# Kernel optimization log

Hardware: AMD Instinct MI355X
Metric: run time of the kernel (lower is better)

## Reference

```python
import jax, jax.numpy as jnp
import numpy as np

H = 2048
B, L, S = 4, 4096, 10

def setup_inputs() -> dict:
    key = jax.random.key(0)
    k1, k2, k3, k4, k5, k6 = jax.random.split(key, 6)
    scale = 1.0 / np.sqrt(H)
    return {
        "h_english": jax.random.normal(k1, (B, L, H), dtype=jnp.float32),
        "h_lojban": jax.random.normal(k2, (B, S, H), dtype=jnp.float32),
        "w_q": jax.random.normal(k3, (H, H), dtype=jnp.float32) * scale,
        "w_k": jax.random.normal(k4, (H, H), dtype=jnp.float32) * scale,
        "w_v": jax.random.normal(k5, (H, H), dtype=jnp.float32) * scale,
        "w_o": jax.random.normal(k6, (H, H), dtype=jnp.float32) * scale,
        "alpha": jnp.float32(0.1),
    }

def reference(h_english, h_lojban, w_q, w_k, w_v, w_o, alpha):
    h = h_english.shape[-1]
    # torch Linear: y = x @ W^T
    q = jnp.einsum('blh,oh->blo', h_english, w_q)   # [B,L,H]
    k = jnp.einsum('bsh,oh->bso', h_lojban, w_k)    # [B,S,H]
    v = jnp.einsum('bsh,oh->bso', h_lojban, w_v)    # [B,S,H]
    scores = jnp.einsum('blh,bsh->bls', q, k) / jnp.sqrt(jnp.float32(h))  # [B,L,S]
    probs = jax.nn.softmax(scores, axis=-1)
    context = jnp.einsum('bls,bsh->blh', probs, v)  # [B,L,H]
    delta = jnp.einsum('blh,oh->blo', context, w_o)
    return h_english + alpha * delta
```

## Files before the change

kernel.cpp:

```cpp
#include <hip/hip_runtime.h>

#define SDIM 10
#define HDIM 2048
#define LDIM 4096
#define BDIM 4

#define KSCALE 0.02209708691207961f

__global__ __launch_bounds__(256) void kv_kernel(
    const float* __restrict__ h_l, const float* __restrict__ w_k,
    const float* __restrict__ w_v, float* __restrict__ k_out,
    float* __restrict__ v_out) {
  const int b = blockIdx.y;
  const int wave = threadIdx.x >> 6;
  const int lane = threadIdx.x & 63;
  const int opair = blockIdx.x * 4 + wave;
  const int o0 = opair * 2;

  const float4* hl4 = (const float4*)(h_l + (size_t)b * SDIM * HDIM);
  const float4* wk0 = (const float4*)(w_k + (size_t)o0 * HDIM);
  const float4* wk1 = (const float4*)(w_k + (size_t)(o0 + 1) * HDIM);
  const float4* wv0 = (const float4*)(w_v + (size_t)o0 * HDIM);
  const float4* wv1 = (const float4*)(w_v + (size_t)(o0 + 1) * HDIM);

  float ak0[SDIM], ak1[SDIM], av0[SDIM], av1[SDIM];
#pragma unroll
  for (int s = 0; s < SDIM; s++) { ak0[s] = ak1[s] = av0[s] = av1[s] = 0.f; }

#pragma unroll
  for (int j = 0; j < 8; j++) {
    const int idx = j * 64 + lane;
    const float4 a0 = wk0[idx], a1 = wk1[idx];
    const float4 c0 = wv0[idx], c1 = wv1[idx];
#pragma unroll
    for (int s = 0; s < SDIM; s++) {
      const float4 h = hl4[s * 512 + idx];
      ak0[s] += a0.x * h.x + a0.y * h.y + a0.z * h.z + a0.w * h.w;
      ak1[s] += a1.x * h.x + a1.y * h.y + a1.z * h.z + a1.w * h.w;
      av0[s] += c0.x * h.x + c0.y * h.y + c0.z * h.z + c0.w * h.w;
      av1[s] += c1.x * h.x + c1.y * h.y + c1.z * h.z + c1.w * h.w;
    }
  }
#pragma unroll
  for (int s = 0; s < SDIM; s++) {
#pragma unroll
    for (int d = 1; d < 64; d <<= 1) {
      ak0[s] += __shfl_xor(ak0[s], d);
      ak1[s] += __shfl_xor(ak1[s], d);
      av0[s] += __shfl_xor(av0[s], d);
      av1[s] += __shfl_xor(av1[s], d);
    }
  }
  if (lane == 0) {
#pragma unroll
    for (int s = 0; s < SDIM; s++) {
      const size_t base = ((size_t)b * SDIM + s) * HDIM + o0;
      k_out[base]     = ak0[s];
      k_out[base + 1] = ak1[s];
      v_out[base]     = av0[s];
      v_out[base + 1] = av1[s];
    }
  }
}

#define OSPLIT 16
__global__ __launch_bounds__(256) void kk_part_kernel(
    const float* __restrict__ k_in, const float* __restrict__ w_q,
    float* __restrict__ part) {
  const int b = blockIdx.z;
  const int oc = blockIdx.y >> 1;
  const int s0 = (blockIdx.y & 1) * 5;
  const int f4 = blockIdx.x * 256 + threadIdx.x;

  __shared__ float ksh[5 * 128];
  for (int idx = threadIdx.x; idx < 5 * 128; idx += 256) {
    const int s = idx >> 7, oo = idx & 127;
    ksh[idx] = k_in[((size_t)b * SDIM + s0 + s) * HDIM + oc * 128 + oo];
  }
  __syncthreads();

  float4 acc[5];
#pragma unroll
  for (int s = 0; s < 5; s++) acc[s] = make_float4(0.f, 0.f, 0.f, 0.f);

  const float4* wq4 = (const float4*)w_q;
  for (int oo = 0; oo < 128; oo++) {
    const float4 w = wq4[(size_t)(oc * 128 + oo) * 512 + f4];
#pragma unroll
    for (int s = 0; s < 5; s++) {
      const float kv = ksh[s * 128 + oo];
      acc[s].x += kv * w.x; acc[s].y += kv * w.y;
      acc[s].z += kv * w.z; acc[s].w += kv * w.w;
    }
  }
#pragma unroll
  for (int s = 0; s < 5; s++) {
    ((float4*)part)[(((size_t)oc * BDIM + b) * SDIM + s0 + s) * 512 + f4] = acc[s];
  }
}

__global__ __launch_bounds__(256) void kk_reduce_kernel(
    const float* __restrict__ part, float* __restrict__ kk_out) {
  const int t = blockIdx.x * 256 + threadIdx.x;
  const float4* p4 = (const float4*)part;
  float4 acc = make_float4(0.f, 0.f, 0.f, 0.f);
#pragma unroll
  for (int p = 0; p < OSPLIT; p++) {
    const float4 v = p4[(size_t)p * 20480 + t];
    acc.x += v.x; acc.y += v.y; acc.z += v.z; acc.w += v.w;
  }
  ((float4*)kk_out)[t] = acc;
}

__global__ __launch_bounds__(256) void vo_kernel(
    const float* __restrict__ v_in, const float* __restrict__ w_o,
    float* __restrict__ vo_out) {
  const int b = blockIdx.y;
  const int wave = threadIdx.x >> 6;
  const int lane = threadIdx.x & 63;
  const int opair = blockIdx.x * 4 + wave;
  const int o0 = opair * 2;

  const float4* vb4 = (const float4*)(v_in + (size_t)b * SDIM * HDIM);
  const float4* wo0 = (const float4*)(w_o + (size_t)o0 * HDIM);
  const float4* wo1 = (const float4*)(w_o + (size_t)(o0 + 1) * HDIM);

  float a0[SDIM], a1[SDIM];
#pragma unroll
  for (int s = 0; s < SDIM; s++) { a0[s] = a1[s] = 0.f; }

#pragma unroll
  for (int j = 0; j < 8; j++) {
    const int idx = j * 64 + lane;
    const float4 w0 = wo0[idx], w1 = wo1[idx];
#pragma unroll
    for (int s = 0; s < SDIM; s++) {
      const float4 h = vb4[s * 512 + idx];
      a0[s] += w0.x * h.x + w0.y * h.y + w0.z * h.z + w0.w * h.w;
      a1[s] += w1.x * h.x + w1.y * h.y + w1.z * h.z + w1.w * h.w;
    }
  }
#pragma unroll
  for (int s = 0; s < SDIM; s++) {
#pragma unroll
    for (int d = 1; d < 64; d <<= 1) {
      a0[s] += __shfl_xor(a0[s], d);
      a1[s] += __shfl_xor(a1[s], d);
    }
  }
  if (lane == 0) {
#pragma unroll
    for (int s = 0; s < SDIM; s++) {
      const size_t base = ((size_t)b * SDIM + s) * HDIM + o0;
      vo_out[base]     = a0[s];
      vo_out[base + 1] = a1[s];
    }
  }
}

__global__ __launch_bounds__(256) void attn_kernel(
    const float* __restrict__ h_e, const float* __restrict__ kk,
    const float* __restrict__ vo, const float* __restrict__ alpha_p,
    float* __restrict__ out) {
  const int b = blockIdx.y;
  const int wave = threadIdx.x >> 6;
  const int lane = threadIdx.x & 63;
  const int row0 = blockIdx.x * 8 + wave * 2;
  const float alpha = *alpha_p;
  const float4* kkb = (const float4*)(kk + (size_t)b * SDIM * HDIM);
  const float4* vob = (const float4*)(vo + (size_t)b * SDIM * HDIM);
  const size_t rowbase = ((size_t)b * LDIM + row0) * HDIM;

  float4 he[2][8];
#pragma unroll
  for (int r = 0; r < 2; r++) {
    const float4* src = (const float4*)(h_e + rowbase + (size_t)r * HDIM);
#pragma unroll
    for (int i = 0; i < 8; i++) he[r][i] = src[i * 64 + lane];
  }

  float acc[2][SDIM];
#pragma unroll
  for (int r = 0; r < 2; r++)
#pragma unroll
    for (int s = 0; s < SDIM; s++) acc[r][s] = 0.f;

#pragma unroll
  for (int i = 0; i < 8; i++) {
#pragma unroll
    for (int s = 0; s < SDIM; s++) {
      const float4 kv = kkb[s * 512 + i * 64 + lane];
#pragma unroll
      for (int r = 0; r < 2; r++)
        acc[r][s] += he[r][i].x * kv.x + he[r][i].y * kv.y +
                     he[r][i].z * kv.z + he[r][i].w * kv.w;
    }
  }

#pragma unroll
  for (int r = 0; r < 2; r++)
#pragma unroll
    for (int s = 0; s < SDIM; s++) {
      float v = acc[r][s];
      v += __shfl_xor(v, 1);
      v += __shfl_xor(v, 2);
      v += __shfl_xor(v, 4);
      v += __shfl_xor(v, 8);
      v += __shfl_xor(v, 16);
      v += __shfl_xor(v, 32);
      acc[r][s] = v * KSCALE;
    }

#pragma unroll
  for (int r = 0; r < 2; r++) {
    float m = acc[r][0];
#pragma unroll
    for (int s = 1; s < SDIM; s++) m = fmaxf(m, acc[r][s]);
    float sum = 0.f;
#pragma unroll
    for (int s = 0; s < SDIM; s++) {
      acc[r][s] = __expf(acc[r][s] - m);
      sum += acc[r][s];
    }
    const float inv = alpha / sum;
#pragma unroll
    for (int s = 0; s < SDIM; s++) acc[r][s] *= inv;
  }

#pragma unroll
  for (int i = 0; i < 8; i++) {
    float4 o4[2];
#pragma unroll
    for (int r = 0; r < 2; r++) o4[r] = he[r][i];
#pragma unroll
    for (int s = 0; s < SDIM; s++) {
      const float4 vv = vob[s * 512 + i * 64 + lane];
#pragma unroll
      for (int r = 0; r < 2; r++) {
        o4[r].x += acc[r][s] * vv.x;
        o4[r].y += acc[r][s] * vv.y;
        o4[r].z += acc[r][s] * vv.z;
        o4[r].w += acc[r][s] * vv.w;
      }
    }
#pragma unroll
    for (int r = 0; r < 2; r++)
      ((float4*)(out + rowbase + (size_t)r * HDIM))[i * 64 + lane] = o4[r];
  }
}

extern "C" void kernel_launch(void* const* d_in, const int* in_sizes, int n_in,
                              void* d_out, int out_size, void* d_ws, size_t ws_size,
                              hipStream_t stream) {
  const float* h_e   = (const float*)d_in[0];
  const float* h_l   = (const float*)d_in[1];
  const float* w_q   = (const float*)d_in[2];
  const float* w_k   = (const float*)d_in[3];
  const float* w_v   = (const float*)d_in[4];
  const float* w_o   = (const float*)d_in[5];
  const float* alpha = (const float*)d_in[6];
  float* out = (float*)d_out;

  float* ws      = (float*)d_ws;
  float* k_ws    = ws;
  float* v_ws    = ws + 81920;
  float* kk_ws   = ws + 163840;
  float* vo_ws   = ws + 245760;
  float* part_ws = ws + 327680;

  kv_kernel<<<dim3(256, BDIM), 256, 0, stream>>>(h_l, w_k, w_v, k_ws, v_ws);
  kk_part_kernel<<<dim3(2, 32, BDIM), 256, 0, stream>>>(k_ws, w_q, part_ws);
  vo_kernel<<<dim3(256, BDIM), 256, 0, stream>>>(v_ws, w_o, vo_ws);
  kk_reduce_kernel<<<80, 256, 0, stream>>>(part_ws, kk_ws);
  attn_kernel<<<dim3(512, BDIM), 256, 0, stream>>>(h_e, kk_ws, vo_ws, alpha, out);
}
```

Before: 417.8 us.

## Batch-merge KV/VO projections and stage attention K/V chunks through LDS

The kv and vo kernels now compute one output column for all four batches per wave instead of two columns for one batch. Each weight row is read once rather than once per batch, which cuts weight traffic. The attention kernel stages the kk and vo vectors into double-buffered LDS with global_load_lds and block-level barriers, replacing the per-wave redundant global loads. This adds synchronisation and LDS pressure, and the larger accumulator arrays raise register use.

New measurement: 556.9 us. 33.3% more time.

```diff
diff --git a/kernel.cpp b/kernel.cpp
--- a/kernel.cpp
+++ b/kernel.cpp
@@ -7,59 +7,57 @@
 
 #define KSCALE 0.02209708691207961f
 
-__global__ __launch_bounds__(256) void kv_kernel(
+__global__ __launch_bounds__(256, 2) void kv_kernel(
     const float* __restrict__ h_l, const float* __restrict__ w_k,
     const float* __restrict__ w_v, float* __restrict__ k_out,
     float* __restrict__ v_out) {
-  const int b = blockIdx.y;
   const int wave = threadIdx.x >> 6;
   const int lane = threadIdx.x & 63;
-  const int opair = blockIdx.x * 4 + wave;
-  const int o0 = opair * 2;
-
-  const float4* hl4 = (const float4*)(h_l + (size_t)b * SDIM * HDIM);
-  const float4* wk0 = (const float4*)(w_k + (size_t)o0 * HDIM);
-  const float4* wk1 = (const float4*)(w_k + (size_t)(o0 + 1) * HDIM);
-  const float4* wv0 = (const float4*)(w_v + (size_t)o0 * HDIM);
-  const float4* wv1 = (const float4*)(w_v + (size_t)(o0 + 1) * HDIM);
-
-  float ak0[SDIM], ak1[SDIM], av0[SDIM], av1[SDIM];
-#pragma unroll
-  for (int s = 0; s < SDIM; s++) { ak0[s] = ak1[s] = av0[s] = av1[s] = 0.f; }
+  const int o = blockIdx.x * 4 + wave;
+
+  const float4* wk = (const float4*)(w_k + (size_t)o * HDIM);
+  const float4* wv = (const float4*)(w_v + (size_t)o * HDIM);
+  const float4* hl4 = (const float4*)h_l;
+
+  float ak[BDIM][SDIM], av[BDIM][SDIM];
+#pragma unroll
+  for (int b = 0; b < BDIM; b++)
+#pragma unroll
+    for (int s = 0; s < SDIM; s++) { ak[b][s] = 0.f; av[b][s] = 0.f; }
 
 #pragma unroll
   for (int j = 0; j < 8; j++) {
     const int idx = j * 64 + lane;
-    const float4 a0 = wk0[idx], a1 = wk1[idx];
-    const float4 c0 = wv0[idx], c1 = wv1[idx];
+    const float4 a = wk[idx];
+    const float4 c = wv[idx];
+#pragma unroll
+    for (int b = 0; b < BDIM; b++)
+#pragma unroll
+      for (int s = 0; s < SDIM; s++) {
+        const float4 h = hl4[(size_t)(b * SDIM + s) * 512 + idx];
+        ak[b][s] += a.x * h.x + a.y * h.y + a.z * h.z + a.w * h.w;
+        av[b][s] += c.x * h.x + c.y * h.y + c.z * h.z + c.w * h.w;
+      }
+  }
+#pragma unroll
+  for (int b = 0; b < BDIM; b++)
 #pragma unroll
     for (int s = 0; s < SDIM; s++) {
-      const float4 h = hl4[s * 512 + idx];
-      ak0[s] += a0.x * h.x + a0.y * h.y + a0.z * h.z + a0.w * h.w;
-      ak1[s] += a1.x * h.x + a1.y * h.y + a1.z * h.z + a1.w * h.w;
-      av0[s] += c0.x * h.x + c0.y * h.y + c0.z * h.z + c0.w * h.w;
-      av1[s] += c1.x * h.x + c1.y * h.y + c1.z * h.z + c1.w * h.w;
-    }
-  }
-#pragma unroll
-  for (int s = 0; s < SDIM; s++) {
-#pragma unroll
-    for (int d = 1; d < 64; d <<= 1) {
-      ak0[s] += __shfl_xor(ak0[s], d);
-      ak1[s] += __shfl_xor(ak1[s], d);
-      av0[s] += __shfl_xor(av0[s], d);
-      av1[s] += __shfl_xor(av1[s], d);
-    }
-  }
+#pragma unroll
+      for (int d = 1; d < 64; d <<= 1) {
+        ak[b][s] += __shfl_xor(ak[b][s], d);
+        av[b][s] += __shfl_xor(av[b][s], d);
+      }
+    }
   if (lane == 0) {
 #pragma unroll
-    for (int s = 0; s < SDIM; s++) {
-      const size_t base = ((size_t)b * SDIM + s) * HDIM + o0;
-      k_out[base]     = ak0[s];
-      k_out[base + 1] = ak1[s];
-      v_out[base]     = av0[s];
-      v_out[base + 1] = av1[s];
-    }
+    for (int b = 0; b < BDIM; b++)
+#pragma unroll
+      for (int s = 0; s < SDIM; s++) {
+        const size_t base = ((size_t)b * SDIM + s) * HDIM + o;
+        k_out[base] = ak[b][s];
+        v_out[base] = av[b][s];
+      }
   }
 }
 
@@ -112,65 +110,80 @@
   ((float4*)kk_out)[t] = acc;
 }
 
-__global__ __launch_bounds__(256) void vo_kernel(
+__global__ __launch_bounds__(256, 2) void vo_kernel(
     const float* __restrict__ v_in, const float* __restrict__ w_o,
     float* __restrict__ vo_out) {
-  const int b = blockIdx.y;
   const int wave = threadIdx.x >> 6;
   const int lane = threadIdx.x & 63;
-  const int opair = blockIdx.x * 4 + wave;
-  const int o0 = opair * 2;
-
-  const float4* vb4 = (const float4*)(v_in + (size_t)b * SDIM * HDIM);
-  const float4* wo0 = (const float4*)(w_o + (size_t)o0 * HDIM);
-  const float4* wo1 = (const float4*)(w_o + (size_t)(o0 + 1) * HDIM);
-
-  float a0[SDIM], a1[SDIM];
-#pragma unroll
-  for (int s = 0; s < SDIM; s++) { a0[s] = a1[s] = 0.f; }
+  const int o = blockIdx.x * 4 + wave;
+
+  const float4* wo = (const float4*)(w_o + (size_t)o * HDIM);
+  const float4* vb4 = (const float4*)v_in;
+
+  float a[BDIM][SDIM];
+#pragma unroll
+  for (int b = 0; b < BDIM; b++)
+#pragma unroll
+    for (int s = 0; s < SDIM; s++) a[b][s] = 0.f;
 
 #pragma unroll
   for (int j = 0; j < 8; j++) {
     const int idx = j * 64 + lane;
-    const float4 w0 = wo0[idx], w1 = wo1[idx];
+    const float4 w = wo[idx];
+#pragma unroll
+    for (int b = 0; b < BDIM; b++)
+#pragma unroll
+      for (int s = 0; s < SDIM; s++) {
+        const float4 h = vb4[(size_t)(b * SDIM + s) * 512 + idx];
+        a[b][s] += w.x * h.x + w.y * h.y + w.z * h.z + w.w * h.w;
+      }
+  }
+#pragma unroll
+  for (int b = 0; b < BDIM; b++)
 #pragma unroll
     for (int s = 0; s < SDIM; s++) {
-      const float4 h = vb4[s * 512 + idx];
-      a0[s] += w0.x * h.x + w0.y * h.y + w0.z * h.z + w0.w * h.w;
-      a1[s] += w1.x * h.x + w1.y * h.y + w1.z * h.z + w1.w * h.w;
-    }
-  }
-#pragma unroll
-  for (int s = 0; s < SDIM; s++) {
-#pragma unroll
-    for (int d = 1; d < 64; d <<= 1) {
-      a0[s] += __shfl_xor(a0[s], d);
-      a1[s] += __shfl_xor(a1[s], d);
-    }
-  }
+#pragma unroll
+      for (int d = 1; d < 64; d <<= 1) a[b][s] += __shfl_xor(a[b][s], d);
+    }
   if (lane == 0) {
 #pragma unroll
-    for (int s = 0; s < SDIM; s++) {
-      const size_t base = ((size_t)b * SDIM + s) * HDIM + o0;
-      vo_out[base]     = a0[s];
-      vo_out[base + 1] = a1[s];
-    }
-  }
-}
-
-__global__ __launch_bounds__(256) void attn_kernel(
+    for (int b = 0; b < BDIM; b++)
+#pragma unroll
+      for (int s = 0; s < SDIM; s++)
+        vo_out[((size_t)b * SDIM + s) * HDIM + o] = a[b][s];
+  }
+}
+
+__device__ __forceinline__ void stage_chunk(const float4* __restrict__ src,
+                                            float4* lds_base, int j, int tid,
+                                            int wave) {
+#pragma unroll
+  for (int k = 0; k < 5; k++) {
+    const int idx = k * 256 + tid;
+    const float4* g = src + (size_t)(idx >> 7) * 512 + j * 128 + (idx & 127);
+    float4* l = lds_base + k * 256 + (wave << 6);
+    __builtin_amdgcn_global_load_lds(
+        (const __attribute__((address_space(1))) void*)g,
+        (__attribute__((address_space(3))) void*)l, 16, 0, 0);
+  }
+}
+
+__global__ __launch_bounds__(256, 3) void attn_kernel(
     const float* __restrict__ h_e, const float* __restrict__ kk,
     const float* __restrict__ vo, const float* __restrict__ alpha_p,
     float* __restrict__ out) {
   const int b = blockIdx.y;
   const int wave = threadIdx.x >> 6;
   const int lane = threadIdx.x & 63;
+  const int tid = threadIdx.x;
   const int row0 = blockIdx.x * 8 + wave * 2;
   const float alpha = *alpha_p;
   const float4* kkb = (const float4*)(kk + (size_t)b * SDIM * HDIM);
   const float4* vob = (const float4*)(vo + (size_t)b * SDIM * HDIM);
   const size_t rowbase = ((size_t)b * LDIM + row0) * HDIM;
 
+  __shared__ float4 lds[2][SDIM * 128];
+
   float4 he[2][8];
 #pragma unroll
   for (int r = 0; r < 2; r++) {
@@ -185,15 +198,23 @@
 #pragma unroll
     for (int s = 0; s < SDIM; s++) acc[r][s] = 0.f;
 
-#pragma unroll
-  for (int i = 0; i < 8; i++) {
-#pragma unroll
-    for (int s = 0; s < SDIM; s++) {
-      const float4 kv = kkb[s * 512 + i * 64 + lane];
-#pragma unroll
-      for (int r = 0; r < 2; r++)
-        acc[r][s] += he[r][i].x * kv.x + he[r][i].y * kv.y +
-                     he[r][i].z * kv.z + he[r][i].w * kv.w;
+  stage_chunk(kkb, lds[0], 0, tid, wave);
+#pragma unroll
+  for (int j = 0; j < 4; j++) {
+    __syncthreads();
+    if (j < 3) stage_chunk(kkb, lds[(j + 1) & 1], j + 1, tid, wave);
+    const float4* buf = lds[j & 1];
+#pragma unroll
+    for (int ii = 0; ii < 2; ii++) {
+      const int i = j * 2 + ii;
+#pragma unroll
+      for (int s = 0; s < SDIM; s++) {
+        const float4 kv = buf[s * 128 + ii * 64 + lane];
+#pragma unroll
+        for (int r = 0; r < 2; r++)
+          acc[r][s] += he[r][i].x * kv.x + he[r][i].y * kv.y +
+                       he[r][i].z * kv.z + he[r][i].w * kv.w;
+      }
     }
   }
 
@@ -210,7 +231,6 @@
       v += __shfl_xor(v, 32);
       acc[r][s] = v * KSCALE;
     }
-
 #pragma unroll
   for (int r = 0; r < 2; r++) {
     float m = acc[r][0];
@@ -227,25 +247,33 @@
     for (int s = 0; s < SDIM; s++) acc[r][s] *= inv;
   }
 
-#pragma unroll
-  for (int i = 0; i < 8; i++) {
-    float4 o4[2];
-#pragma unroll
-    for (int r = 0; r < 2; r++) o4[r] = he[r][i];
-#pragma unroll
-    for (int s = 0; s < SDIM; s++) {
-      const float4 vv = vob[s * 512 + i * 64 + lane];
-#pragma unroll
-      for (int r = 0; r < 2; r++) {
-        o4[r].x += acc[r][s] * vv.x;
-        o4[r].y += acc[r][s] * vv.y;
-        o4[r].z += acc[r][s] * vv.z;
-        o4[r].w += acc[r][s] * vv.w;
-      }
-    }
-#pragma unroll
-    for (int r = 0; r < 2; r++)
-      ((float4*)(out + rowbase + (size_t)r * HDIM))[i * 64 + lane] = o4[r];
+  stage_chunk(vob, lds[0], 0, tid, wave);
+#pragma unroll
+  for (int j = 0; j < 4; j++) {
+    __syncthreads();
+    if (j < 3) stage_chunk(vob, lds[(j + 1) & 1], j + 1, tid, wave);
+    const float4* buf = lds[j & 1];
+#pragma unroll
+    for (int ii = 0; ii < 2; ii++) {
+      const int i = j * 2 + ii;
+      float4 o4[2];
+#pragma unroll
+      for (int r = 0; r < 2; r++) o4[r] = he[r][i];
+#pragma unroll
+      for (int s = 0; s < SDIM; s++) {
+        const float4 vv = buf[s * 128 + ii * 64 + lane];
+#pragma unroll
+        for (int r = 0; r < 2; r++) {
+          o4[r].x += acc[r][s] * vv.x;
+          o4[r].y += acc[r][s] * vv.y;
+          o4[r].z += acc[r][s] * vv.z;
+          o4[r].w += acc[r][s] * vv.w;
+        }
+      }
+#pragma unroll
+      for (int r = 0; r < 2; r++)
+        ((float4*)(out + rowbase + (size_t)r * HDIM))[i * 64 + lane] = o4[r];
+    }
   }
 }
 
@@ -268,9 +296,9 @@
   float* vo_ws   = ws + 245760;
   float* part_ws = ws + 327680;
 
-  kv_kernel<<<dim3(256, BDIM), 256, 0, stream>>>(h_l, w_k, w_v, k_ws, v_ws);
+  kv_kernel<<<512, 256, 0, stream>>>(h_l, w_k, w_v, k_ws, v_ws);
   kk_part_kernel<<<dim3(2, 32, BDIM), 256, 0, stream>>>(k_ws, w_q, part_ws);
-  vo_kernel<<<dim3(256, BDIM), 256, 0, stream>>>(v_ws, w_o, vo_ws);
+  vo_kernel<<<512, 256, 0, stream>>>(v_ws, w_o, vo_ws);
   kk_reduce_kernel<<<80, 256, 0, stream>>>(part_ws, kk_ws);
   attn_kernel<<<dim3(512, BDIM), 256, 0, stream>>>(h_e, kk_ws, vo_ws, alpha, out);
 }
```
